# Performance work log

Measured on AMD Instinct MI355X. Metric: run time of the kernel, lower is better.

## Reference

```python
import jax, jax.numpy as jnp
import numpy as np

N_NODES = 20000
N_EDGES = 320000
D_IN = 32      # raw node feature dim
D = 128        # hidden_dim / d
DV = 16        # per-head dim
NV = 8         # num heads (NV*DV == D)
D_OUT = 8      # action-space size
N_LAYERS = 2


def _lin(k, fi, fo, scale=0.02):
    return jax.random.normal(k, (fi, fo), jnp.float32) * scale


def setup_inputs() -> dict:
    key = jax.random.key(0)
    ks = jax.random.split(key, 32)
    inp = {
        "x": jax.random.normal(ks[0], (N_NODES, D_IN), jnp.float32),
        "edge_index": jax.random.randint(ks[1], (2, N_EDGES), 0, N_NODES, dtype=jnp.int64),
        # embedding MLP
        "W1": _lin(ks[2], D_IN, D), "b1": jnp.zeros((D,), jnp.float32),
        "W2": _lin(ks[3], D, D),    "b2": jnp.zeros((D,), jnp.float32),
        # output head
        "Wout": _lin(ks[4], D, D_OUT), "bout": jnp.zeros((D_OUT,), jnp.float32),
    }
    # per-layer attention params: W_target, W_source, hidden_embedding (D -> NV*DV), out (DV -> D)
    for l in range(N_LAYERS):
        base = 5 + 4 * l
        inp[f"Wt{l}"] = _lin(ks[base + 0], D, NV * DV); inp[f"bt{l}"] = jnp.zeros((NV * DV,), jnp.float32)
        inp[f"Ws{l}"] = _lin(ks[base + 1], D, NV * DV); inp[f"bs{l}"] = jnp.zeros((NV * DV,), jnp.float32)
        inp[f"Wh{l}"] = _lin(ks[base + 2], D, NV * DV); inp[f"bh{l}"] = jnp.zeros((NV * DV,), jnp.float32)
        inp[f"Wo{l}"] = _lin(ks[base + 3], DV, D);      inp[f"bo{l}"] = jnp.zeros((D,), jnp.float32)
    return inp


def _gat_layer(h, src, dst, Wt, bt, Ws, bs, Wh, bh, Wo, bo):
    E = src.shape[0]
    # gather + project (relu), view as [E, nv, dv]
    ht = jax.nn.relu(h[dst] @ Wt + bt).reshape(E, NV, DV)   # x_i / target
    hs = jax.nn.relu(h[src] @ Ws + bs).reshape(E, NV, DV)   # x_j / source
    e = jnp.sum(ht * hs, axis=-1)                           # [E, nv] per-head logits
    # numerically stable segment softmax over edges sharing a target node
    m = jax.ops.segment_max(e, dst, num_segments=N_NODES)   # [N, nv]
    ex = jnp.exp(e - m[dst])
    s = jax.ops.segment_sum(ex, dst, num_segments=N_NODES) + 1e-12
    alpha = ex / s[dst]                                     # [E, nv]
    hn = jax.nn.relu(h[src] @ Wh + bh).reshape(E, NV, DV)
    msg = jnp.mean(hn * alpha[:, :, None], axis=1)          # [E, dv] (mean over heads)
    agg = jax.ops.segment_sum(msg, dst, num_segments=N_NODES)  # aggr='add'
    return jax.nn.relu(agg @ Wo + bo)                       # [N, d_out=D]


def reference(x, edge_index, W1, b1, W2, b2, Wout, bout,
              Wt0, bt0, Ws0, bs0, Wh0, bh0, Wo0, bo0,
              Wt1, bt1, Ws1, bs1, Wh1, bh1, Wo1, bo1):
    # Embedding MLP
    h = jax.nn.relu(x @ W1 + b1)
    h = jax.nn.relu(h @ W2 + b2)
    # add self loops once (matches add_self_loops applied per layer)
    loops = jnp.arange(N_NODES, dtype=edge_index.dtype)
    src = jnp.concatenate([edge_index[0], loops])
    dst = jnp.concatenate([edge_index[1], loops])
    h = _gat_layer(h, src, dst, Wt0, bt0, Ws0, bs0, Wh0, bh0, Wo0, bo0)
    h = _gat_layer(h, src, dst, Wt1, bt1, Ws1, bs1, Wh1, bh1, Wo1, bo1)
    return h @ Wout + bout                                  # [N, output_dim]
```

## Files before the change

kernel.cpp:

```cpp
#include <hip/hip_runtime.h>
#include <hip/hip_fp16.h>

#define N_NODES 20000
#define N_EDGES 320000
#define E_TOT   (N_EDGES + N_NODES)
#define D       128
#define D_OUT   8
#define MAXDEG  64
#define NTILE   (N_NODES / 16)
#define MLP_BLOCKS 313
#define BUCKET_BLOCKS ((E_TOT + 255) / 256)

typedef _Float16 f16x8 __attribute__((ext_vector_type(8)));
typedef float    f32x4 __attribute__((ext_vector_type(4)));

__device__ __forceinline__ void split8(const float* v, f16x8& hi, f16x8& lo) {
#pragma unroll
    for (int e = 0; e < 8; ++e) {
        _Float16 h = (_Float16)v[e];
        hi[e] = h; lo[e] = (_Float16)(v[e] - (float)h);
    }
}

__global__ void prep_kernel(const float* __restrict__ W1, const float* __restrict__ W2,
                            const float* __restrict__ Wt0, const float* __restrict__ Ws0,
                            const float* __restrict__ Wh0, const float* __restrict__ Wt1,
                            const float* __restrict__ Ws1, const float* __restrict__ Wh1,
                            __half* __restrict__ W1c, __half* __restrict__ W2c,
                            __half* __restrict__ Wc2, int* __restrict__ cnt) {
    const int b = blockIdx.x, tid = threadIdx.x;
    if (b < 79) {
        int i = b * 256 + tid;
        if (i < N_NODES) cnt[i] = 0;
        return;
    }
    if (b < 143) {
        int idx = (b - 79) * 256 + tid;
        if (idx < 4096) {
            int c = idx >> 5, k = idx & 31;
            W1c[c * 32 + k] = __float2half(W1[k * D + c]);
        }
        int c = idx >> 7, k = idx & 127;
        W2c[c * 128 + k] = __float2half(W2[k * D + c]);
        return;
    }
    int bb = b - 143;
    int l = bb / 192, r = bb % 192, m = r / 64, kp = r % 64;
    int k = kp * 2 + (tid >> 7), c = tid & 127;
    const float* W = (l == 0) ? (m == 0 ? Wt0 : m == 1 ? Ws0 : Wh0)
                              : (m == 0 ? Wt1 : m == 1 ? Ws1 : Wh1);
    Wc2[l * 49152 + (m * 128 + c) * 128 + k] = __float2half(W[(size_t)k * D + c]);
}

__global__ __launch_bounds__(256) void build_fwd(
        const int* __restrict__ ei, int* __restrict__ cnt, int* __restrict__ slots,
        const float* __restrict__ x,
        const __half* __restrict__ W1c, const __half* __restrict__ W2c,
        const float* __restrict__ b1, const float* __restrict__ b2,
        const __half* __restrict__ Wc0,
        const float* __restrict__ bt, const float* __restrict__ bs,
        const float* __restrict__ bh,
        float* __restrict__ pt0, __half* __restrict__ psn0) {
    if (blockIdx.x >= MLP_BLOCKS) {
        int e = (blockIdx.x - MLP_BLOCKS) * 256 + threadIdx.x;
        if (e < E_TOT) {
            int src, dst;
            if (e < N_EDGES) { src = ei[e]; dst = ei[N_EDGES + e]; }
            else             { src = dst = e - N_EDGES; }
            int pos = atomicAdd(&cnt[dst], 1);
            if (pos < MAXDEG) slots[dst * MAXDEG + pos] = src;
        }
        return;
    }
    __shared__ __half hHi[4][16][136];
    __shared__ __half hLo[4][16][136];
    const int tb   = blockIdx.x;
    const int tid  = threadIdx.x;
    const int lane = tid & 63, wv = tid >> 6;
    const int cl   = lane & 15, kg = (lane >> 4) * 8;
    const int rj   = (lane >> 4) * 4;
    const int tg   = min(tb * 4 + wv, NTILE - 1);

    {
        const int row = tg * 16 + cl;
        float tmp[8];
        *(float4*)tmp       = *(const float4*)(x + (size_t)row * 32 + kg);
        *(float4*)(tmp + 4) = *(const float4*)(x + (size_t)row * 32 + kg + 4);
        f16x8 aH, aL; split8(tmp, aH, aL);
        f32x4 acc[8];
#pragma unroll
        for (int ct = 0; ct < 8; ++ct) acc[ct] = (f32x4){0.f, 0.f, 0.f, 0.f};
#pragma unroll
        for (int ct = 0; ct < 8; ++ct) {
            const f16x8 bf = *(const f16x8*)(W1c + (size_t)(ct * 16 + cl) * 32 + kg);
            acc[ct] = __builtin_amdgcn_mfma_f32_16x16x32_f16(aH, bf, acc[ct], 0, 0, 0);
            acc[ct] = __builtin_amdgcn_mfma_f32_16x16x32_f16(aL, bf, acc[ct], 0, 0, 0);
        }
#pragma unroll
        for (int ct = 0; ct < 8; ++ct) {
            const float bb = b1[ct * 16 + cl];
#pragma unroll
            for (int j = 0; j < 4; ++j) {
                float v = fmaxf(acc[ct][j] + bb, 0.f);
                _Float16 h = (_Float16)v;
                ((_Float16*)&hHi[wv][rj + j][ct * 16 + cl])[0] = h;
                ((_Float16*)&hLo[wv][rj + j][ct * 16 + cl])[0] = (_Float16)(v - (float)h);
            }
        }
    }
    __syncthreads();
    {
        f16x8 aH[4], aL[4];
#pragma unroll
        for (int ks = 0; ks < 4; ++ks) {
            aH[ks] = *(const f16x8*)&hHi[wv][cl][ks * 32 + kg];
            aL[ks] = *(const f16x8*)&hLo[wv][cl][ks * 32 + kg];
        }
        f32x4 acc[8];
#pragma unroll
        for (int ct = 0; ct < 8; ++ct) acc[ct] = (f32x4){0.f, 0.f, 0.f, 0.f};
#pragma unroll
        for (int ks = 0; ks < 4; ++ks)
#pragma unroll
            for (int ct = 0; ct < 8; ++ct) {
                const f16x8 bf = *(const f16x8*)(W2c + (size_t)(ct * 16 + cl) * 128 + ks * 32 + kg);
                acc[ct] = __builtin_amdgcn_mfma_f32_16x16x32_f16(aH[ks], bf, acc[ct], 0, 0, 0);
                acc[ct] = __builtin_amdgcn_mfma_f32_16x16x32_f16(aL[ks], bf, acc[ct], 0, 0, 0);
            }
        __syncthreads();
#pragma unroll
        for (int ct = 0; ct < 8; ++ct) {
            const float bb = b2[ct * 16 + cl];
#pragma unroll
            for (int j = 0; j < 4; ++j) {
                float v = fmaxf(acc[ct][j] + bb, 0.f);
                _Float16 h = (_Float16)v;
                ((_Float16*)&hHi[wv][rj + j][ct * 16 + cl])[0] = h;
                ((_Float16*)&hLo[wv][rj + j][ct * 16 + cl])[0] = (_Float16)(v - (float)h);
            }
        }
    }
    __syncthreads();
    const int ctl[6] = {2 * wv, 2 * wv + 1, 8 + 2 * wv, 9 + 2 * wv, 16 + 2 * wv, 17 + 2 * wv};
    f16x8 bf[6][4];
#pragma unroll
    for (int i = 0; i < 6; ++i)
#pragma unroll
        for (int ks = 0; ks < 4; ++ks)
            bf[i][ks] = *(const f16x8*)(Wc0 + (size_t)(ctl[i] * 16 + cl) * 128 + ks * 32 + kg);

    __half2* psn2 = (__half2*)psn0;
    for (int rt = 0; rt < 4; ++rt) {
        const int tg2 = min(tb * 4 + rt, NTILE - 1);
        f16x8 aH[4], aL[4];
#pragma unroll
        for (int ks = 0; ks < 4; ++ks) {
            aH[ks] = *(const f16x8*)&hHi[rt][cl][ks * 32 + kg];
            aL[ks] = *(const f16x8*)&hLo[rt][cl][ks * 32 + kg];
        }
        f32x4 acc[6];
#pragma unroll
        for (int i = 0; i < 6; ++i) acc[i] = (f32x4){0.f, 0.f, 0.f, 0.f};
#pragma unroll
        for (int i = 0; i < 6; ++i)
#pragma unroll
            for (int ks = 0; ks < 4; ++ks) {
                acc[i] = __builtin_amdgcn_mfma_f32_16x16x32_f16(aH[ks], bf[i][ks], acc[i], 0, 0, 0);
                acc[i] = __builtin_amdgcn_mfma_f32_16x16x32_f16(aL[ks], bf[i][ks], acc[i], 0, 0, 0);
            }
        const int rbase = tg2 * 16 + rj;
#pragma unroll
        for (int i = 0; i < 2; ++i) {
            const int c = ctl[i] * 16 + cl;
            const float bb = bt[c];
#pragma unroll
            for (int j = 0; j < 4; ++j)
                pt0[(size_t)(rbase + j) * D + c] = fmaxf(acc[i][j] + bb, 0.f);
        }
#pragma unroll
        for (int p = 0; p < 2; ++p) {
            const int c = (ctl[2 + p] - 8) * 16 + cl;
            const float bS = bs[c], bN = bh[c];
#pragma unroll
            for (int j = 0; j < 4; ++j) {
                float vS = fmaxf(acc[2 + p][j] + bS, 0.f);
                float vN = fmaxf(acc[4 + p][j] + bN, 0.f);
                psn2[(size_t)(rbase + j) * 128 + c] = __floats2half2_rn(vS, vN);
            }
        }
    }
}

#define LDV(kk) (*(const uint4*)(psn + (size_t)__shfl(sv, hbase + (kk)) * 256 + 8 * l32))

#define PROC(v, kk) {                                                     \
    const float2 p0 = __half22float2(*(const __half2*)&(v).x);            \
    const float2 p1 = __half22float2(*(const __half2*)&(v).y);            \
    const float2 p2 = __half22float2(*(const __half2*)&(v).z);            \
    const float2 p3 = __half22float2(*(const __half2*)&(v).w);            \
    float d_ = ptv.x * p0.x + ptv.y * p1.x + ptv.z * p2.x + ptv.w * p3.x; \
    d_ += __shfl_xor(d_, 1);                                              \
    d_ += __shfl_xor(d_, 2);                                              \
    const float ex_ = (base + (kk) < len) ? __expf(d_) : 0.f;             \
    sA += ex_; M0 += ex_ * p0.y; M1 += ex_ * p1.y;                        \
    M2 += ex_ * p2.y; M3 += ex_ * p3.y; }

__device__ __forceinline__ void gat_node(
        const float* __restrict__ pt, const __half* __restrict__ psn,
        const int* __restrict__ cnt, const int* __restrict__ slots,
        const float* __restrict__ Wo, const float* __restrict__ bo,
        int node, int l32, int hbase, float hv[4]) {
    const float4 ptv = *(const float4*)(pt + (size_t)node * D + 4 * l32);
    const int len = min(cnt[node], MAXDEG);
    const int maxlen = max(len, __shfl_xor(len, 32));
    const int e0 = node * MAXDEG;

    float sA = 0.f, M0 = 0.f, M1 = 0.f, M2 = 0.f, M3 = 0.f;
    for (int base = 0; base < maxlen; base += 32) {
        const int sv = slots[e0 + min(base + l32, len - 1)];
        const int kmax = min(32, maxlen - base);
        uint4 va = LDV(0);
        uint4 vb = LDV(min(1, kmax - 1));
        uint4 vc = LDV(min(2, kmax - 1));
        uint4 vd = LDV(min(3, kmax - 1));
        for (int k = 0; k < kmax; k += 4) {
            const int kn = k + 4;
            uint4 wa = LDV(min(kn,     kmax - 1));
            uint4 wb = LDV(min(kn + 1, kmax - 1));
            uint4 wc = LDV(min(kn + 2, kmax - 1));
            uint4 wd = LDV(min(kn + 3, kmax - 1));
            PROC(va, k); PROC(vb, k + 1); PROC(vc, k + 2); PROC(vd, k + 3);
            va = wa; vb = wb; vc = wc; vd = wd;
        }
    }
    const float inv = 1.f / (sA + 1e-12f);
    float av[4] = {M0 * inv, M1 * inv, M2 * inv, M3 * inv};
#pragma unroll
    for (int j = 0; j < 4; ++j) {
        av[j] += __shfl_xor(av[j], 4);
        av[j] += __shfl_xor(av[j], 8);
        av[j] += __shfl_xor(av[j], 16);
        av[j] *= 0.125f;
    }
    float a0 = bo[l32], a1 = bo[l32 + 32], a2 = bo[l32 + 64], a3 = bo[l32 + 96];
#pragma unroll
    for (int k = 0; k < 16; ++k) {
        const float val = __shfl(av[k & 3], hbase + (k >> 2));
        a0 += val * Wo[k * D + l32];
        a1 += val * Wo[k * D + l32 + 32];
        a2 += val * Wo[k * D + l32 + 64];
        a3 += val * Wo[k * D + l32 + 96];
    }
    hv[0] = fmaxf(a0, 0.f); hv[1] = fmaxf(a1, 0.f);
    hv[2] = fmaxf(a2, 0.f); hv[3] = fmaxf(a3, 0.f);
}

__global__ __launch_bounds__(512) void attn0_kernel(
        const float* __restrict__ pt0, const __half* __restrict__ psn0,
        const int* __restrict__ cnt, const int* __restrict__ slots,
        const float* __restrict__ Wo, const float* __restrict__ bo,
        const __half* __restrict__ Wc1,
        const float* __restrict__ bt, const float* __restrict__ bs,
        const float* __restrict__ bh,
        float* __restrict__ pt1, __half* __restrict__ psn1) {
    __shared__ float h2s[16][132];
    const int tid  = threadIdx.x;
    const int lane = tid & 63;
    const int l32  = lane & 31;
    const int hbase = lane & 32;
    const int nidx = tid >> 5;
    const int node = blockIdx.x * 16 + nidx;

    float hv[4];
    gat_node(pt0, psn0, cnt, slots, Wo, bo, node, l32, hbase, hv);
    h2s[nidx][l32]      = hv[0];
    h2s[nidx][l32 + 32] = hv[1];
    h2s[nidx][l32 + 64] = hv[2];
    h2s[nidx][l32 + 96] = hv[3];

    const int w_ = tid >> 6;
    const int cl = lane & 15, kg = (lane >> 4) * 8;
    f16x8 bT[4], bS[4], bN[4];
#pragma unroll
    for (int ks = 0; ks < 4; ++ks) {
        bT[ks] = *(const f16x8*)(Wc1 + (size_t)((w_)      * 16 + cl) * 128 + ks * 32 + kg);
        bS[ks] = *(const f16x8*)(Wc1 + (size_t)((8 + w_)  * 16 + cl) * 128 + ks * 32 + kg);
        bN[ks] = *(const f16x8*)(Wc1 + (size_t)((16 + w_) * 16 + cl) * 128 + ks * 32 + kg);
    }
    __syncthreads();

    f16x8 aH[4], aL[4];
#pragma unroll
    for (int ks = 0; ks < 4; ++ks) {
        float tmp[8];
        *(float4*)tmp       = *(const float4*)&h2s[cl][ks * 32 + kg];
        *(float4*)(tmp + 4) = *(const float4*)&h2s[cl][ks * 32 + kg + 4];
        split8(tmp, aH[ks], aL[ks]);
    }
    f32x4 accT = {0.f,0.f,0.f,0.f}, accS = {0.f,0.f,0.f,0.f}, accN = {0.f,0.f,0.f,0.f};
#pragma unroll
    for (int ks = 0; ks < 4; ++ks) {
        accT = __builtin_amdgcn_mfma_f32_16x16x32_f16(aH[ks], bT[ks], accT, 0, 0, 0);
        accT = __builtin_amdgcn_mfma_f32_16x16x32_f16(aL[ks], bT[ks], accT, 0, 0, 0);
        accS = __builtin_amdgcn_mfma_f32_16x16x32_f16(aH[ks], bS[ks], accS, 0, 0, 0);
        accS = __builtin_amdgcn_mfma_f32_16x16x32_f16(aL[ks], bS[ks], accS, 0, 0, 0);
        accN = __builtin_amdgcn_mfma_f32_16x16x32_f16(aH[ks], bN[ks], accN, 0, 0, 0);
        accN = __builtin_amdgcn_mfma_f32_16x16x32_f16(aL[ks], bN[ks], accN, 0, 0, 0);
    }
    const int rbase = blockIdx.x * 16 + (lane >> 4) * 4;
    const int c = w_ * 16 + cl;
    const float bbT = bt[c], bbS = bs[c], bbN = bh[c];
    __half2* psn2 = (__half2*)psn1;
#pragma unroll
    for (int j = 0; j < 4; ++j) {
        pt1[(size_t)(rbase + j) * D + c] = fmaxf(accT[j] + bbT, 0.f);
        float vS = fmaxf(accS[j] + bbS, 0.f);
        float vN = fmaxf(accN[j] + bbN, 0.f);
        psn2[(size_t)(rbase + j) * 128 + c] = __floats2half2_rn(vS, vN);
    }
}

__global__ __launch_bounds__(512) void attn1_kernel(
        const float* __restrict__ pt1, const __half* __restrict__ psn1,
        const int* __restrict__ cnt, const int* __restrict__ slots,
        const float* __restrict__ Wo, const float* __restrict__ bo,
        const float* __restrict__ Wout, const float* __restrict__ bout,
        float* __restrict__ outp) {
    const int tid  = threadIdx.x;
    const int lane = tid & 63;
    const int l32  = lane & 31;
    const int hbase = lane & 32;
    const int node = blockIdx.x * 16 + (tid >> 5);

    float hv[4];
    gat_node(pt1, psn1, cnt, slots, Wo, bo, node, l32, hbase, hv);

    float po[8];
#pragma unroll
    for (int o = 0; o < 8; ++o)
        po[o] = hv[0] * Wout[l32 * D_OUT + o] + hv[1] * Wout[(l32 + 32) * D_OUT + o]
              + hv[2] * Wout[(l32 + 64) * D_OUT + o] + hv[3] * Wout[(l32 + 96) * D_OUT + o];
#pragma unroll
    for (int m = 1; m < 32; m <<= 1) {
#pragma unroll
        for (int o = 0; o < 8; ++o) po[o] += __shfl_xor(po[o], m);
    }
    if (l32 == 0) {
#pragma unroll
        for (int o = 0; o < 8; ++o)
            outp[(size_t)node * D_OUT + o] = po[o] + bout[o];
    }
}

extern "C" void kernel_launch(void* const* d_in, const int* in_sizes, int n_in,
                              void* d_out, int out_size, void* d_ws, size_t ws_size,
                              hipStream_t stream) {
    const float* x    = (const float*)d_in[0];
    const int*   ei   = (const int*)  d_in[1];
    const float* W1   = (const float*)d_in[2];
    const float* b1   = (const float*)d_in[3];
    const float* W2   = (const float*)d_in[4];
    const float* b2   = (const float*)d_in[5];
    const float* Wout = (const float*)d_in[6];
    const float* bout = (const float*)d_in[7];
    float* out = (float*)d_out;

    float*  pt0  = (float*)d_ws;
    float*  pt1  = pt0 + (size_t)N_NODES * D;
    __half* psn0 = (__half*)(pt1 + (size_t)N_NODES * D);
    __half* psn1 = psn0 + (size_t)N_NODES * 256;
    __half* W1c  = psn1 + (size_t)N_NODES * 256;
    __half* W2c  = W1c + 128 * 32;
    __half* Wc2  = W2c + 128 * 128;
    int* cnt   = (int*)(Wc2 + 2 * 384 * 128);
    int* slots = cnt + N_NODES;

    prep_kernel<<<527, 256, 0, stream>>>(
        W1, W2,
        (const float*)d_in[8],  (const float*)d_in[10], (const float*)d_in[12],
        (const float*)d_in[16], (const float*)d_in[18], (const float*)d_in[20],
        W1c, W2c, Wc2, cnt);

    build_fwd<<<MLP_BLOCKS + BUCKET_BLOCKS, 256, 0, stream>>>(
        ei, cnt, slots, x, W1c, W2c, b1, b2,
        Wc2,
        (const float*)d_in[9], (const float*)d_in[11], (const float*)d_in[13],
        pt0, psn0);

    attn0_kernel<<<NTILE, 512, 0, stream>>>(
        pt0, psn0, cnt, slots,
        (const float*)d_in[14], (const float*)d_in[15],
        Wc2 + 49152,
        (const float*)d_in[17], (const float*)d_in[19], (const float*)d_in[21],
        pt1, psn1);

    attn1_kernel<<<NTILE, 512, 0, stream>>>(
        pt1, psn1, cnt, slots,
        (const float*)d_in[22], (const float*)d_in[23],
        Wout, bout, out);
}
```

Before: 95.70 us.

## Store target projections in fp16, use fdot2 for logits, transpose Wo

Stores the per-node target projection pt in fp16 rather than fp32, which halves its write and read traffic. psn is re-laid out so source pairs and hidden-embedding pairs sit in adjacent halves, letting the attention logit use packed fp16 dot2 instructions instead of unpacking to float. Wo is pre-transposed in the prep kernel so each lane reads it with float4 loads. The cost is lower precision in the logits, and psn is now written with scattered half-word stores instead of packed half2 stores.

```diff
diff --git a/kernel.cpp b/kernel.cpp
--- a/kernel.cpp
+++ b/kernel.cpp
@@ -12,6 +12,7 @@
 #define BUCKET_BLOCKS ((E_TOT + 255) / 256)
 
 typedef _Float16 f16x8 __attribute__((ext_vector_type(8)));
+typedef _Float16 h2v   __attribute__((ext_vector_type(2)));
 typedef float    f32x4 __attribute__((ext_vector_type(4)));
 
 __device__ __forceinline__ void split8(const float* v, f16x8& hi, f16x8& lo) {
@@ -20,14 +21,27 @@
         _Float16 h = (_Float16)v[e];
         hi[e] = h; lo[e] = (_Float16)(v[e] - (float)h);
     }
+}
+
+__device__ __forceinline__ float dot2(unsigned int a, unsigned int b, float c) {
+#if __has_builtin(__builtin_amdgcn_fdot2)
+    return __builtin_amdgcn_fdot2(__builtin_bit_cast(h2v, a),
+                                  __builtin_bit_cast(h2v, b), c, false);
+#else
+    const float2 fa = __half22float2(__builtin_bit_cast(__half2, a));
+    const float2 fb = __half22float2(__builtin_bit_cast(__half2, b));
+    return c + fa.x * fb.x + fa.y * fb.y;
+#endif
 }
 
 __global__ void prep_kernel(const float* __restrict__ W1, const float* __restrict__ W2,
                             const float* __restrict__ Wt0, const float* __restrict__ Ws0,
                             const float* __restrict__ Wh0, const float* __restrict__ Wt1,
                             const float* __restrict__ Ws1, const float* __restrict__ Wh1,
+                            const float* __restrict__ Wo0, const float* __restrict__ Wo1,
                             __half* __restrict__ W1c, __half* __restrict__ W2c,
-                            __half* __restrict__ Wc2, int* __restrict__ cnt) {
+                            __half* __restrict__ Wc2, float* __restrict__ WoT,
+                            int* __restrict__ cnt) {
     const int b = blockIdx.x, tid = threadIdx.x;
     if (b < 79) {
         int i = b * 256 + tid;
@@ -44,12 +58,21 @@
         W2c[c * 128 + k] = __float2half(W2[k * D + c]);
         return;
     }
-    int bb = b - 143;
-    int l = bb / 192, r = bb % 192, m = r / 64, kp = r % 64;
-    int k = kp * 2 + (tid >> 7), c = tid & 127;
-    const float* W = (l == 0) ? (m == 0 ? Wt0 : m == 1 ? Ws0 : Wh0)
-                              : (m == 0 ? Wt1 : m == 1 ? Ws1 : Wh1);
-    Wc2[l * 49152 + (m * 128 + c) * 128 + k] = __float2half(W[(size_t)k * D + c]);
+    if (b < 527) {
+        int bb = b - 143;
+        int l = bb / 192, r = bb % 192, m = r / 64, kp = r % 64;
+        int k = kp * 2 + (tid >> 7), c = tid & 127;
+        const float* W = (l == 0) ? (m == 0 ? Wt0 : m == 1 ? Ws0 : Wh0)
+                                  : (m == 0 ? Wt1 : m == 1 ? Ws1 : Wh1);
+        Wc2[l * 49152 + (m * 128 + c) * 128 + k] = __float2half(W[(size_t)k * D + c]);
+        return;
+    }
+    int bb = b - 527;
+    int l = bb >> 3;
+    int i = (bb & 7) * 256 + tid;
+    int c = i >> 4, k = i & 15;
+    const float* Wo = l == 0 ? Wo0 : Wo1;
+    WoT[l * 2048 + i] = Wo[k * D + c];
 }
 
 __global__ __launch_bounds__(256) void build_fwd(
@@ -60,7 +83,7 @@
         const __half* __restrict__ Wc0,
         const float* __restrict__ bt, const float* __restrict__ bs,
         const float* __restrict__ bh,
-        float* __restrict__ pt0, __half* __restrict__ psn0) {
+        __half* __restrict__ pt0, __half* __restrict__ psn0) {
     if (blockIdx.x >= MLP_BLOCKS) {
         int e = (blockIdx.x - MLP_BLOCKS) * 256 + threadIdx.x;
         if (e < E_TOT) {
@@ -149,7 +172,6 @@
         for (int ks = 0; ks < 4; ++ks)
             bf[i][ks] = *(const f16x8*)(Wc0 + (size_t)(ctl[i] * 16 + cl) * 128 + ks * 32 + kg);
 
-    __half2* psn2 = (__half2*)psn0;
     for (int rt = 0; rt < 4; ++rt) {
         const int tg2 = min(tb * 4 + rt, NTILE - 1);
         f16x8 aH[4], aL[4];
@@ -175,17 +197,18 @@
             const float bb = bt[c];
 #pragma unroll
             for (int j = 0; j < 4; ++j)
-                pt0[(size_t)(rbase + j) * D + c] = fmaxf(acc[i][j] + bb, 0.f);
+                pt0[(size_t)(rbase + j) * D + c] = __float2half(fmaxf(acc[i][j] + bb, 0.f));
         }
 #pragma unroll
         for (int p = 0; p < 2; ++p) {
             const int c = (ctl[2 + p] - 8) * 16 + cl;
+            const int qb = ((c >> 1) << 2) + (c & 1);
             const float bS = bs[c], bN = bh[c];
 #pragma unroll
             for (int j = 0; j < 4; ++j) {
-                float vS = fmaxf(acc[2 + p][j] + bS, 0.f);
-                float vN = fmaxf(acc[4 + p][j] + bN, 0.f);
-                psn2[(size_t)(rbase + j) * 128 + c] = __floats2half2_rn(vS, vN);
+                __half* prow = psn0 + (size_t)(rbase + j) * 256;
+                prow[qb]     = __float2half(fmaxf(acc[2 + p][j] + bS, 0.f));
+                prow[qb + 2] = __float2half(fmaxf(acc[4 + p][j] + bN, 0.f));
             }
         }
     }
@@ -194,23 +217,21 @@
 #define LDV(kk) (*(const uint4*)(psn + (size_t)__shfl(sv, hbase + (kk)) * 256 + 8 * l32))
 
 #define PROC(v, kk) {                                                     \
-    const float2 p0 = __half22float2(*(const __half2*)&(v).x);            \
-    const float2 p1 = __half22float2(*(const __half2*)&(v).y);            \
-    const float2 p2 = __half22float2(*(const __half2*)&(v).z);            \
-    const float2 p3 = __half22float2(*(const __half2*)&(v).w);            \
-    float d_ = ptv.x * p0.x + ptv.y * p1.x + ptv.z * p2.x + ptv.w * p3.x; \
+    float d_ = dot2((v).x, ptu.x, dot2((v).z, ptu.y, 0.f));               \
     d_ += __shfl_xor(d_, 1);                                              \
     d_ += __shfl_xor(d_, 2);                                              \
     const float ex_ = (base + (kk) < len) ? __expf(d_) : 0.f;             \
-    sA += ex_; M0 += ex_ * p0.y; M1 += ex_ * p1.y;                        \
-    M2 += ex_ * p2.y; M3 += ex_ * p3.y; }
+    const float2 q0 = __half22float2(__builtin_bit_cast(__half2, (v).y)); \
+    const float2 q1 = __half22float2(__builtin_bit_cast(__half2, (v).w)); \
+    sA += ex_; M0 += ex_ * q0.x; M1 += ex_ * q0.y;                        \
+    M2 += ex_ * q1.x; M3 += ex_ * q1.y; }
 
 __device__ __forceinline__ void gat_node(
-        const float* __restrict__ pt, const __half* __restrict__ psn,
+        const __half* __restrict__ pth, const __half* __restrict__ psn,
         const int* __restrict__ cnt, const int* __restrict__ slots,
-        const float* __restrict__ Wo, const float* __restrict__ bo,
+        const float* __restrict__ WoT, const float* __restrict__ bo,
         int node, int l32, int hbase, float hv[4]) {
-    const float4 ptv = *(const float4*)(pt + (size_t)node * D + 4 * l32);
+    const uint2 ptu = *(const uint2*)(pth + (size_t)node * D + 4 * l32);
     const int len = min(cnt[node], MAXDEG);
     const int maxlen = max(len, __shfl_xor(len, 32));
     const int e0 = node * MAXDEG;
@@ -243,26 +264,33 @@
         av[j] *= 0.125f;
     }
     float a0 = bo[l32], a1 = bo[l32 + 32], a2 = bo[l32 + 64], a3 = bo[l32 + 96];
-#pragma unroll
-    for (int k = 0; k < 16; ++k) {
-        const float val = __shfl(av[k & 3], hbase + (k >> 2));
-        a0 += val * Wo[k * D + l32];
-        a1 += val * Wo[k * D + l32 + 32];
-        a2 += val * Wo[k * D + l32 + 64];
-        a3 += val * Wo[k * D + l32 + 96];
+    const float4* w0 = (const float4*)(WoT + (size_t)(l32)      * 16);
+    const float4* w1 = (const float4*)(WoT + (size_t)(l32 + 32) * 16);
+    const float4* w2 = (const float4*)(WoT + (size_t)(l32 + 64) * 16);
+    const float4* w3 = (const float4*)(WoT + (size_t)(l32 + 96) * 16);
+#pragma unroll
+    for (int q = 0; q < 4; ++q) {
+        const float4 c0 = w0[q], c1 = w1[q], c2 = w2[q], c3 = w3[q];
+#pragma unroll
+        for (int j = 0; j < 4; ++j) {
+            const int k = q * 4 + j;
+            const float val = __shfl(av[k & 3], hbase + (k >> 2));
+            a0 += val * (&c0.x)[j]; a1 += val * (&c1.x)[j];
+            a2 += val * (&c2.x)[j]; a3 += val * (&c3.x)[j];
+        }
     }
     hv[0] = fmaxf(a0, 0.f); hv[1] = fmaxf(a1, 0.f);
     hv[2] = fmaxf(a2, 0.f); hv[3] = fmaxf(a3, 0.f);
 }
 
 __global__ __launch_bounds__(512) void attn0_kernel(
-        const float* __restrict__ pt0, const __half* __restrict__ psn0,
+        const __half* __restrict__ pt0, const __half* __restrict__ psn0,
         const int* __restrict__ cnt, const int* __restrict__ slots,
-        const float* __restrict__ Wo, const float* __restrict__ bo,
+        const float* __restrict__ WoT, const float* __restrict__ bo,
         const __half* __restrict__ Wc1,
         const float* __restrict__ bt, const float* __restrict__ bs,
         const float* __restrict__ bh,
-        float* __restrict__ pt1, __half* __restrict__ psn1) {
+        __half* __restrict__ pt1, __half* __restrict__ psn1) {
     __shared__ float h2s[16][132];
     const int tid  = threadIdx.x;
     const int lane = tid & 63;
@@ -272,7 +300,7 @@
     const int node = blockIdx.x * 16 + nidx;
 
     float hv[4];
-    gat_node(pt0, psn0, cnt, slots, Wo, bo, node, l32, hbase, hv);
+    gat_node(pt0, psn0, cnt, slots, WoT, bo, node, l32, hbase, hv);
     h2s[nidx][l32]      = hv[0];
     h2s[nidx][l32 + 32] = hv[1];
     h2s[nidx][l32 + 64] = hv[2];
@@ -309,21 +337,21 @@
     }
     const int rbase = blockIdx.x * 16 + (lane >> 4) * 4;
     const int c = w_ * 16 + cl;
+    const int qb = ((c >> 1) << 2) + (c & 1);
     const float bbT = bt[c], bbS = bs[c], bbN = bh[c];
-    __half2* psn2 = (__half2*)psn1;
 #pragma unroll
     for (int j = 0; j < 4; ++j) {
-        pt1[(size_t)(rbase + j) * D + c] = fmaxf(accT[j] + bbT, 0.f);
-        float vS = fmaxf(accS[j] + bbS, 0.f);
-        float vN = fmaxf(accN[j] + bbN, 0.f);
-        psn2[(size_t)(rbase + j) * 128 + c] = __floats2half2_rn(vS, vN);
+        pt1[(size_t)(rbase + j) * D + c] = __float2half(fmaxf(accT[j] + bbT, 0.f));
+        __half* prow = psn1 + (size_t)(rbase + j) * 256;
+        prow[qb]     = __float2half(fmaxf(accS[j] + bbS, 0.f));
+        prow[qb + 2] = __float2half(fmaxf(accN[j] + bbN, 0.f));
     }
 }
 
 __global__ __launch_bounds__(512) void attn1_kernel(
-        const float* __restrict__ pt1, const __half* __restrict__ psn1,
+        const __half* __restrict__ pt1, const __half* __restrict__ psn1,
         const int* __restrict__ cnt, const int* __restrict__ slots,
-        const float* __restrict__ Wo, const float* __restrict__ bo,
+        const float* __restrict__ WoT, const float* __restrict__ bo,
         const float* __restrict__ Wout, const float* __restrict__ bout,
         float* __restrict__ outp) {
     const int tid  = threadIdx.x;
@@ -333,7 +361,7 @@
     const int node = blockIdx.x * 16 + (tid >> 5);
 
     float hv[4];
-    gat_node(pt1, psn1, cnt, slots, Wo, bo, node, l32, hbase, hv);
+    gat_node(pt1, psn1, cnt, slots, WoT, bo, node, l32, hbase, hv);
 
     float po[8];
 #pragma unroll
@@ -365,21 +393,23 @@
     const float* bout = (const float*)d_in[7];
     float* out = (float*)d_out;
 
-    float*  pt0  = (float*)d_ws;
-    float*  pt1  = pt0 + (size_t)N_NODES * D;
-    __half* psn0 = (__half*)(pt1 + (size_t)N_NODES * D);
+    __half* pt0  = (__half*)d_ws;
+    __half* pt1  = pt0 + (size_t)N_NODES * D;
+    __half* psn0 = pt1 + (size_t)N_NODES * D;
     __half* psn1 = psn0 + (size_t)N_NODES * 256;
     __half* W1c  = psn1 + (size_t)N_NODES * 256;
     __half* W2c  = W1c + 128 * 32;
     __half* Wc2  = W2c + 128 * 128;
-    int* cnt   = (int*)(Wc2 + 2 * 384 * 128);
+    float*  WoT  = (float*)(Wc2 + 2 * 384 * 128);
+    int* cnt   = (int*)(WoT + 2 * 2048);
     int* slots = cnt + N_NODES;
 
-    prep_kernel<<<527, 256, 0, stream>>>(
+    prep_kernel<<<543, 256, 0, stream>>>(
         W1, W2,
         (const float*)d_in[8],  (const float*)d_in[10], (const float*)d_in[12],
         (const float*)d_in[16], (const float*)d_in[18], (const float*)d_in[20],
-        W1c, W2c, Wc2, cnt);
+        (const float*)d_in[14], (const float*)d_in[22],
+        W1c, W2c, Wc2, WoT, cnt);
 
     build_fwd<<<MLP_BLOCKS + BUCKET_BLOCKS, 256, 0, stream>>>(
         ei, cnt, slots, x, W1c, W2c, b1, b2,
@@ -389,13 +419,13 @@
 
     attn0_kernel<<<NTILE, 512, 0, stream>>>(
         pt0, psn0, cnt, slots,
-        (const float*)d_in[14], (const float*)d_in[15],
+        WoT, (const float*)d_in[15],
         Wc2 + 49152,
         (const float*)d_in[17], (const float*)d_in[19], (const float*)d_in[21],
         pt1, psn1);
 
     attn1_kernel<<<NTILE, 512, 0, stream>>>(
         pt1, psn1, cnt, slots,
-        (const float*)d_in[22], (const float*)d_in[23],
+        WoT + 2048, (const float*)d_in[23],
         Wout, bout, out);
 }
```

Measured after the change: 101.7 us. 1.06x slower.
